# Performance work log

Measured on AMD Instinct MI355X. Metric: run time of the kernel, lower is better.

The kernel has to match this reference:

```python
import jax, jax.numpy as jnp
import numpy as np
import math

B, S, D, H = 2, 2048, 1024, 16
DK = D // H


def setup_inputs() -> dict:
    key = jax.random.key(0)
    ks = jax.random.split(key, 12)
    sc = 0.02
    inp = {
        "k": jax.random.normal(ks[0], (B, S, D), jnp.float32),
        "q": jax.random.normal(ks[1], (B, S, D), jnp.float32),
        "v": jax.random.normal(ks[2], (B, S, D), jnp.float32),
        "mask": 1,
        "w_k": jax.random.normal(ks[3], (D, D), jnp.float32) * sc,
        "b_k": jax.random.normal(ks[4], (D,), jnp.float32) * sc,
        "w_q": jax.random.normal(ks[5], (D, D), jnp.float32) * sc,
        "b_q": jax.random.normal(ks[6], (D,), jnp.float32) * sc,
        "w_v": jax.random.normal(ks[7], (D, D), jnp.float32) * sc,
        "b_v": jax.random.normal(ks[8], (D,), jnp.float32) * sc,
        "w_o": jax.random.normal(ks[9], (D, D), jnp.float32) * sc,
        "b_o": jax.random.normal(ks[10], (D,), jnp.float32) * sc,
    }
    return inp


def _mha(k, q, v, mask, w_k, b_k, w_q, b_q, w_v, b_v, w_o, b_o):
    # torch Linear: x @ W.T + b  (W is [out, in])
    key = k @ w_k.T + b_k
    query = q @ w_q.T + b_q
    value = v @ w_v.T + b_v
    # [B, S, D] -> [B, H, S, DK]
    key = key.reshape(B, S, H, DK).transpose(0, 2, 1, 3)
    query = query.reshape(B, S, H, DK).transpose(0, 2, 1, 3)
    value = value.reshape(B, S, H, DK).transpose(0, 2, 1, 3)
    # NOTE: original multiplies by sqrt(d_k) (not divides) -- faithful.
    scores = jnp.einsum("bhqd,bhkd->bhqk", query, key) * math.sqrt(DK)
    if mask:
        causal = jnp.triu(jnp.ones((S, S), dtype=bool), k=1)
        scores = jnp.where(causal, -jnp.inf, scores)
    # dropout p=0.0 is identity (original applies dropout to scores pre-softmax)
    attn = jax.nn.softmax(scores, axis=-1)
    out = jnp.einsum("bhqk,bhkd->bhqd", attn, value)
    out = out.transpose(0, 2, 1, 3).reshape(B, S, D)
    return out @ w_o.T + b_o


def reference(k, q, v, mask, w_k, b_k, w_q, b_q, w_v, b_v, w_o, b_o):
    return _mha(k, q, v, mask, w_k, b_k, w_q, b_q, w_v, b_v, w_o, b_o)
```

## Files before the change

kernel.cpp:

```cpp
#include <hip/hip_runtime.h>


typedef float f32x4 __attribute__((ext_vector_type(4)));
typedef float f32x16 __attribute__((ext_vector_type(16)));
typedef unsigned int u32x4 __attribute__((ext_vector_type(4)));
typedef _Float16 f16x8 __attribute__((ext_vector_type(8)));
typedef __fp16 fp16x2 __attribute__((ext_vector_type(2)));

#define DEV static __device__ __forceinline__

DEV unsigned short f2h(float x) {
  _Float16 h = (_Float16)x;
  union { _Float16 h; unsigned short u; } v; v.h = h;
  return v.u;
}

DEV unsigned pkrtz(float a, float b) {
  union { fp16x2 h; unsigned u; } v;
  v.h = __builtin_amdgcn_cvt_pkrtz(a, b);
  return v.u;
}

DEV float fexp2(float x) { return __builtin_amdgcn_exp2f(x); }

DEV void pswap(unsigned& a, unsigned& b) {
  auto r = __builtin_amdgcn_permlane32_swap(a, b, false, false);
  a = r[0]; b = r[1];
}

DEV void swap_pair(float v, float& x, float& y) {
  union { float f; unsigned u; } in; in.f = v;
  auto r = __builtin_amdgcn_permlane32_swap(in.u, in.u, false, false);
  union { unsigned u; float f; } ox, oy; ox.u = r[0]; oy.u = r[1];
  x = ox.f; y = oy.f;
}

DEV f16x8 mkfrag(unsigned a, unsigned b, unsigned c, unsigned d) {
  union { unsigned u[4]; f16x8 v; } z;
  z.u[0] = a; z.u[1] = b; z.u[2] = c; z.u[3] = d;
  return z.v;
}

DEV void mfma16(f32x4& d, u32x4 a, u32x4 b) {
  asm("v_mfma_f32_16x16x32_f16 %0, %1, %2, %0" : "+v"(d) : "v"(a), "v"(b));
}

DEV void gload16(const void* g, void* l) {
  __builtin_amdgcn_global_load_lds(
      (const __attribute__((address_space(1))) unsigned int*)g,
      (__attribute__((address_space(3))) unsigned int*)l, 16, 0, 0);
}

DEV u32x4 cvt8(float4 a, float4 b) {
  union { unsigned short us[8]; u32x4 v; } z;
  z.us[0] = f2h(a.x); z.us[1] = f2h(a.y); z.us[2] = f2h(a.z); z.us[3] = f2h(a.w);
  z.us[4] = f2h(b.x); z.us[5] = f2h(b.y); z.us[6] = f2h(b.z); z.us[7] = f2h(b.w);
  return z.v;
}

#define VMCNT0() asm volatile("s_waitcnt vmcnt(0)" ::: "memory")
#define LGKMCNT0() asm volatile("s_waitcnt lgkmcnt(0)" ::: "memory")
#define NOPG(a,b,c,d)  asm volatile("s_nop 7\n\ts_nop 7" : "+v"(a), "+v"(b), "+v"(c), "+v"(d))

__global__ __launch_bounds__(256) void cvt_w(
    const float* __restrict__ wk, const float* __restrict__ wq,
    const float* __restrict__ wv, const float* __restrict__ wo,
    unsigned short* __restrict__ dst) {
  const int i = (blockIdx.x * 256 + threadIdx.x) * 4;
  const float* src; int off;
  if (i < 1048576)      { src = wk; off = 0; }
  else if (i < 2097152) { src = wq; off = 1048576; }
  else if (i < 3145728) { src = wv; off = 2097152; }
  else                  { src = wo; off = 3145728; }
  float4 val = *(const float4*)(src + (i - off));
  ushort4 o;
  o.x = f2h(val.x); o.y = f2h(val.y); o.z = f2h(val.z); o.w = f2h(val.w);
  *(ushort4*)(dst + i) = o;
}

DEV void proj_body(const float* __restrict__ A, const unsigned short* __restrict__ W,
                   const float* __restrict__ bias, void* __restrict__ out, int mode,
                   float oscale, int m0, int n0) {
  __shared__ alignas(16) char lds_a[2][8192];
  __shared__ alignas(16) char lds_b[2][8192];
  const int t = threadIdx.x;
  const int l = t & 63, g = l >> 4, c = l & 15, w = t >> 6;
  const int wr = w >> 1, wc = w & 1;

  f32x4 acc[4][4] = {};

  const int i0 = t, i1 = t + 256;
  const int ar0 = i0 >> 2, as0 = (i0 & 3) ^ (ar0 & 3);
  const int ar1 = i1 >> 2, as1 = (i1 & 3) ^ (ar1 & 3);
  const float* gaf0 = A + (long)(m0 + ar0) * 1024 + as0 * 8;
  const float* gaf1 = A + (long)(m0 + ar1) * 1024 + as1 * 8;
  const unsigned short* gb0 = W + (long)(n0 + ar0) * 1024 + as0 * 8;
  const unsigned short* gb1 = W + (long)(n0 + ar1) * 1024 + as1 * 8;
  const int lo0 = i0 * 16, lo1 = i1 * 16;

  int aoff[4], boff[4];
#pragma unroll
  for (int i = 0; i < 4; i++) {
    const int ra = (wr << 6) + (i << 4) + c;
    aoff[i] = ra * 64 + ((g << 4) ^ ((ra & 3) << 4));
    const int rb = (wc << 6) + (i << 4) + c;
    boff[i] = rb * 64 + ((g << 4) ^ ((rb & 3) << 4));
  }

  float4 r0a = *(const float4*)(gaf0);
  float4 r0b = *(const float4*)(gaf0 + 4);
  float4 r1a = *(const float4*)(gaf1);
  float4 r1b = *(const float4*)(gaf1 + 4);
  gload16(gb0, lds_b[0] + lo0);
  gload16(gb1, lds_b[0] + lo1);

  for (int kt = 0; kt < 32; kt++) {
    const int cur = kt & 1;
    VMCNT0();
    *(u32x4*)(lds_a[cur] + lo0) = cvt8(r0a, r0b);
    *(u32x4*)(lds_a[cur] + lo1) = cvt8(r1a, r1b);
    if (kt + 1 < 32) {
      const int o = (kt + 1) << 5;
      r0a = *(const float4*)(gaf0 + o);
      r0b = *(const float4*)(gaf0 + o + 4);
      r1a = *(const float4*)(gaf1 + o);
      r1b = *(const float4*)(gaf1 + o + 4);
    }
    LGKMCNT0();
    __builtin_amdgcn_s_barrier();
    if (kt + 1 < 32) {
      gload16(gb0 + ((kt + 1) << 5), lds_b[cur ^ 1] + lo0);
      gload16(gb1 + ((kt + 1) << 5), lds_b[cur ^ 1] + lo1);
    }
    u32x4 af[4], bf[4];
#pragma unroll
    for (int i = 0; i < 4; i++) af[i] = *(const u32x4*)(lds_a[cur] + aoff[i]);
#pragma unroll
    for (int j = 0; j < 4; j++) bf[j] = *(const u32x4*)(lds_b[cur] + boff[j]);
#pragma unroll
    for (int i = 0; i < 4; i++)
#pragma unroll
      for (int j = 0; j < 4; j++)
        mfma16(acc[i][j], af[i], bf[j]);
  }

  NOPG(acc[0][0], acc[0][1], acc[0][2], acc[0][3]);
  NOPG(acc[1][0], acc[1][1], acc[1][2], acc[1][3]);
  NOPG(acc[2][0], acc[2][1], acc[2][2], acc[2][3]);
  NOPG(acc[3][0], acc[3][1], acc[3][2], acc[3][3]);

  if (mode == 1) {
#pragma unroll
    for (int j = 0; j < 4; j++) {
      const int n = n0 + (wc << 6) + (j << 4) + c;
      const float bb = bias[n];
      const int h = n >> 6, d = n & 63;
#pragma unroll
      for (int i = 0; i < 4; i++) {
        const int m = m0 + (wr << 6) + (i << 4) + (g << 2);
        const int b = m >> 11, s = m & 2047;
        ushort4 o;
        o.x = f2h(acc[i][j][0] + bb);
        o.y = f2h(acc[i][j][1] + bb);
        o.z = f2h(acc[i][j][2] + bb);
        o.w = f2h(acc[i][j][3] + bb);
        *(ushort4*)&((unsigned short*)out)[((long)((b << 4) + h) * 64 + d) * 2048 + s] = o;
      }
    }
  } else {
#pragma unroll
    for (int j = 0; j < 4; j++) {
      const int n = n0 + (wc << 6) + (j << 4) + c;
      const float bb = bias[n];
#pragma unroll
      for (int i = 0; i < 4; i++) {
#pragma unroll
        for (int r = 0; r < 4; r++) {
          const int m = m0 + (wr << 6) + (i << 4) + (g << 2) + r;
          const float val = (acc[i][j][r] + bb) * oscale;
          const int b = m >> 11, s = m & 2047;
          const int h = n >> 6, d = n & 63;
          ((unsigned short*)out)[((long)((b << 4) + h) * 2048 + s) * 64 + d] = f2h(val);
        }
      }
    }
  }
}

__global__ __launch_bounds__(256) void gemm_proj(
    const float* kf, const float* qf, const float* vf,
    const unsigned short* wkb, const unsigned short* wqb, const unsigned short* wvb,
    const float* bk, const float* bq, const float* bvv,
    unsigned short* Kp, unsigned short* Qp, unsigned short* VpT) {
  const int bid = blockIdx.x;
  const int n = bid / 96;
  const int gg = bid % 96;
  const int m = gg / 3;
  const int z = gg % 3;
  const float* A = (z == 0) ? kf : (z == 1) ? qf : vf;
  const unsigned short* W = (z == 0) ? wkb : (z == 1) ? wqb : wvb;
  const float* bias = (z == 0) ? bk : (z == 1) ? bq : bvv;
  void* out = (z == 0) ? (void*)Kp : (z == 1) ? (void*)Qp : (void*)VpT;
  const float sc = (z == 1) ? 11.5415603271f : 1.0f;
  proj_body(A, W, bias, out, (z == 2) ? 1 : 0, sc, m << 7, n << 7);
}

__global__ __launch_bounds__(256) void gemm_out(
    const unsigned short* __restrict__ A, const unsigned short* __restrict__ W,
    const float* __restrict__ bias, float* __restrict__ out) {
  __shared__ alignas(16) char lds_a[2][8192];
  __shared__ alignas(16) char lds_b[2][8192];
  const int t = threadIdx.x;
  const int l = t & 63, g = l >> 4, c = l & 15, w = t >> 6;
  const int wr = w >> 1, wc = w & 1;
  const int bid = blockIdx.x;
  const int m0 = (bid & 31) << 7, n0 = (bid >> 5) << 7;

  f32x4 acc[4][4] = {};

  const int i0 = t, i1 = t + 256;
  const int ar0 = i0 >> 2, as0 = (i0 & 3) ^ (ar0 & 3);
  const int ar1 = i1 >> 2, as1 = (i1 & 3) ^ (ar1 & 3);
  const unsigned short* ga0 = A + (long)(m0 + ar0) * 1024 + as0 * 8;
  const unsigned short* ga1 = A + (long)(m0 + ar1) * 1024 + as1 * 8;
  const unsigned short* gb0 = W + (long)(n0 + ar0) * 1024 + as0 * 8;
  const unsigned short* gb1 = W + (long)(n0 + ar1) * 1024 + as1 * 8;
  const int lo0 = i0 * 16, lo1 = i1 * 16;

  int aoff[4], boff[4];
#pragma unroll
  for (int i = 0; i < 4; i++) {
    const int ra = (wr << 6) + (i << 4) + c;
    aoff[i] = ra * 64 + ((g << 4) ^ ((ra & 3) << 4));
    const int rb = (wc << 6) + (i << 4) + c;
    boff[i] = rb * 64 + ((g << 4) ^ ((rb & 3) << 4));
  }

  gload16(ga0, lds_a[0] + lo0);
  gload16(ga1, lds_a[0] + lo1);
  gload16(gb0, lds_b[0] + lo0);
  gload16(gb1, lds_b[0] + lo1);

  for (int kt = 0; kt < 32; kt++) {
    const int cur = kt & 1;
    VMCNT0();
    __builtin_amdgcn_s_barrier();
    if (kt + 1 < 32) {
      gload16(ga0 + ((kt + 1) << 5), lds_a[cur ^ 1] + lo0);
      gload16(ga1 + ((kt + 1) << 5), lds_a[cur ^ 1] + lo1);
      gload16(gb0 + ((kt + 1) << 5), lds_b[cur ^ 1] + lo0);
      gload16(gb1 + ((kt + 1) << 5), lds_b[cur ^ 1] + lo1);
    }
    u32x4 af[4], bf[4];
#pragma unroll
    for (int i = 0; i < 4; i++) af[i] = *(const u32x4*)(lds_a[cur] + aoff[i]);
#pragma unroll
    for (int j = 0; j < 4; j++) bf[j] = *(const u32x4*)(lds_b[cur] + boff[j]);
#pragma unroll
    for (int i = 0; i < 4; i++)
#pragma unroll
      for (int j = 0; j < 4; j++)
        mfma16(acc[i][j], af[i], bf[j]);
  }

  NOPG(acc[0][0], acc[0][1], acc[0][2], acc[0][3]);
  NOPG(acc[1][0], acc[1][1], acc[1][2], acc[1][3]);
  NOPG(acc[2][0], acc[2][1], acc[2][2], acc[2][3]);
  NOPG(acc[3][0], acc[3][1], acc[3][2], acc[3][3]);

#pragma unroll
  for (int j = 0; j < 4; j++) {
    const int n = n0 + (wc << 6) + (j << 4) + c;
    const float bb = bias[n];
#pragma unroll
    for (int i = 0; i < 4; i++) {
#pragma unroll
      for (int r = 0; r < 4; r++) {
        const int m = m0 + (wr << 6) + (i << 4) + (g << 2) + r;
        out[(long)m * 1024 + n] = acc[i][j][r] + bb;
      }
    }
  }
}

__global__ __launch_bounds__(128) void attn_kernel(
    const unsigned short* __restrict__ Qp, const unsigned short* __restrict__ Kp,
    const unsigned short* __restrict__ VpT, unsigned short* __restrict__ O) {
  __shared__ alignas(16) char lds_k[2][8192];
  __shared__ alignas(16) char lds_v[2][8192];

  const int t = threadIdx.x;
  const int lane = t & 63, w = t >> 6;
  const int hi = lane >> 5, c32 = lane & 31;
  const int bh = blockIdx.x;
  const int qt = 31 - (int)blockIdx.y;
  const int qs = (qt << 6) + (w << 5);
  const int ntiles = qt + 1;

  const unsigned short* gk[4]; const unsigned short* gv[4]; int lofs[4];
#pragma unroll
  for (int n = 0; n < 4; n++) {
    const int idx = t + 128 * n;
    const int row = idx >> 3, sl = (idx & 7) ^ (row & 7);
    gk[n] = Kp + ((long)bh * 2048 + row) * 64 + sl * 8;
    gv[n] = VpT + ((long)bh * 64 + row) * 2048 + sl * 8;
    lofs[n] = idx * 16;
  }

  int koff[2][4];
#pragma unroll
  for (int x = 0; x < 2; x++)
#pragma unroll
    for (int y = 0; y < 4; y++) {
      const int row = 32 * x + c32;
      koff[x][y] = row * 128 + ((((y << 1) + hi) << 4) ^ ((row & 7) << 4));
    }

  const unsigned short* qrow = Qp + ((long)bh * 2048 + qs + c32) * 64 + hi * 8;
  f16x8 qf[4];
#pragma unroll
  for (int ks = 0; ks < 4; ks++) qf[ks] = *(const f16x8*)(qrow + ks * 16);

  f32x16 oT0 = {}, oT1 = {};
  float mrun = -1e30f, lrun = 0.f;
  const int qloc = (qs & 63) + c32;

#pragma unroll
  for (int n = 0; n < 4; n++) {
    gload16(gk[n], lds_k[0] + lofs[n]);
    gload16(gv[n], lds_v[0] + lofs[n]);
  }

  for (int tt = 0; tt < ntiles; tt++) {
    const int cur = tt & 1;
    VMCNT0();
    __builtin_amdgcn_s_barrier();
    if (tt + 1 < ntiles) {
      const long kvn = (long)(tt + 1) << 6;
#pragma unroll
      for (int n = 0; n < 4; n++) {
        gload16(gk[n] + kvn * 64, lds_k[cur ^ 1] + lofs[n]);
        gload16(gv[n] + kvn,      lds_v[cur ^ 1] + lofs[n]);
      }
    }

    f32x16 s0 = {}, s1 = {};
    __builtin_amdgcn_s_setprio(1);
#pragma unroll
    for (int ks = 0; ks < 4; ks++) {
      const f16x8 a0 = *(const f16x8*)(lds_k[cur] + koff[0][ks]);
      const f16x8 a1 = *(const f16x8*)(lds_k[cur] + koff[1][ks]);
      s0 = __builtin_amdgcn_mfma_f32_32x32x16_f16(a0, qf[ks], s0, 0, 0, 0);
      s1 = __builtin_amdgcn_mfma_f32_32x32x16_f16(a1, qf[ks], s1, 0, 0, 0);
    }
    __builtin_amdgcn_s_setprio(0);

    if (tt == qt) {
#pragma unroll
      for (int r = 0; r < 16; r++) {
        const int kvc = (r & 3) + 8 * (r >> 2) + 4 * hi;
        if (kvc > qloc)      s0[r] = -1e30f;
        if (kvc + 32 > qloc) s1[r] = -1e30f;
      }
    }

    float tm[16];
#pragma unroll
    for (int r = 0; r < 16; r++) tm[r] = fmaxf(s0[r], s1[r]);
#pragma unroll
    for (int d = 8; d >= 1; d >>= 1)
#pragma unroll
      for (int r = 0; r < 8; r++)
        if (r < d) tm[r] = fmaxf(tm[r], tm[r + d]);
    float x, y;
    swap_pair(tm[0], x, y);
    const float pmax = fmaxf(x, y);

    if (!__all(pmax - mrun <= 8.0f)) {
      const float mnew = fmaxf(mrun, pmax);
      const float corr = fexp2(mrun - mnew);
      mrun = mnew;
      lrun *= corr;
      oT0 *= corr;
      oT1 *= corr;
    }

#pragma unroll
    for (int r = 0; r < 16; r++) {
      s0[r] = fexp2(s0[r] - mrun);
      s1[r] = fexp2(s1[r] - mrun);
    }
    float ts[16];
#pragma unroll
    for (int r = 0; r < 16; r++) ts[r] = s0[r] + s1[r];
#pragma unroll
    for (int d = 8; d >= 1; d >>= 1)
#pragma unroll
      for (int r = 0; r < 8; r++)
        if (r < d) ts[r] = ts[r] + ts[r + d];
    lrun += ts[0];

    unsigned pk[8];
#pragma unroll
    for (int m = 0; m < 8; m++) pk[m] = pkrtz(s0[2 * m], s0[2 * m + 1]);
    pswap(pk[0], pk[2]); pswap(pk[1], pk[3]);
    pswap(pk[4], pk[6]); pswap(pk[5], pk[7]);
    const f16x8 pf0 = mkfrag(pk[0], pk[1], pk[2], pk[3]);
    const f16x8 pf1 = mkfrag(pk[4], pk[5], pk[6], pk[7]);
#pragma unroll
    for (int m = 0; m < 8; m++) pk[m] = pkrtz(s1[2 * m], s1[2 * m + 1]);
    pswap(pk[0], pk[2]); pswap(pk[1], pk[3]);
    pswap(pk[4], pk[6]); pswap(pk[5], pk[7]);
    const f16x8 pf2 = mkfrag(pk[0], pk[1], pk[2], pk[3]);
    const f16x8 pf3 = mkfrag(pk[4], pk[5], pk[6], pk[7]);

    __builtin_amdgcn_s_setprio(1);
    {
      const f16x8 v00 = *(const f16x8*)(lds_v[cur] + koff[0][0]);
      const f16x8 v01 = *(const f16x8*)(lds_v[cur] + koff[0][1]);
      const f16x8 v02 = *(const f16x8*)(lds_v[cur] + koff[0][2]);
      const f16x8 v03 = *(const f16x8*)(lds_v[cur] + koff[0][3]);
      oT0 = __builtin_amdgcn_mfma_f32_32x32x16_f16(v00, pf0, oT0, 0, 0, 0);
      oT0 = __builtin_amdgcn_mfma_f32_32x32x16_f16(v01, pf1, oT0, 0, 0, 0);
      oT0 = __builtin_amdgcn_mfma_f32_32x32x16_f16(v02, pf2, oT0, 0, 0, 0);
      oT0 = __builtin_amdgcn_mfma_f32_32x32x16_f16(v03, pf3, oT0, 0, 0, 0);
      const f16x8 v10 = *(const f16x8*)(lds_v[cur] + koff[1][0]);
      const f16x8 v11 = *(const f16x8*)(lds_v[cur] + koff[1][1]);
      const f16x8 v12 = *(const f16x8*)(lds_v[cur] + koff[1][2]);
      const f16x8 v13 = *(const f16x8*)(lds_v[cur] + koff[1][3]);
      oT1 = __builtin_amdgcn_mfma_f32_32x32x16_f16(v10, pf0, oT1, 0, 0, 0);
      oT1 = __builtin_amdgcn_mfma_f32_32x32x16_f16(v11, pf1, oT1, 0, 0, 0);
      oT1 = __builtin_amdgcn_mfma_f32_32x32x16_f16(v12, pf2, oT1, 0, 0, 0);
      oT1 = __builtin_amdgcn_mfma_f32_32x32x16_f16(v13, pf3, oT1, 0, 0, 0);
    }
    __builtin_amdgcn_s_setprio(0);
  }

  float sx, sy;
  swap_pair(lrun, sx, sy);
  const float inv = 1.0f / (sx + sy);
  const int b = bh >> 4, h = bh & 15;
  const long rowbase = ((long)b * 2048 + qs + c32) * 1024 + (h << 6);
#pragma unroll
  for (int dt = 0; dt < 2; dt++) {
#pragma unroll
    for (int g4 = 0; g4 < 4; g4++) {
      const f32x16& o = dt ? oT1 : oT0;
      uint2 pkd;
      pkd.x = pkrtz(o[4 * g4 + 0] * inv, o[4 * g4 + 1] * inv);
      pkd.y = pkrtz(o[4 * g4 + 2] * inv, o[4 * g4 + 3] * inv);
      *(uint2*)&O[rowbase + 32 * dt + 8 * g4 + 4 * hi] = pkd;
    }
  }
}

extern "C" void kernel_launch(void* const* d_in, const int* in_sizes, int n_in,
                              void* d_out, int out_size, void* d_ws, size_t ws_size,
                              hipStream_t stream) {
  (void)in_sizes; (void)n_in; (void)out_size; (void)ws_size;
  const float* kin = (const float*)d_in[0];
  const float* qin = (const float*)d_in[1];
  const float* vin = (const float*)d_in[2];
  const float* wk  = (const float*)d_in[4];
  const float* bk  = (const float*)d_in[5];
  const float* wq  = (const float*)d_in[6];
  const float* bq  = (const float*)d_in[7];
  const float* wv  = (const float*)d_in[8];
  const float* bv  = (const float*)d_in[9];
  const float* wo  = (const float*)d_in[10];
  const float* bo  = (const float*)d_in[11];

  unsigned short* ws  = (unsigned short*)d_ws;
  unsigned short* wkb = ws + 12582912;
  unsigned short* wqb = ws + 13631488;
  unsigned short* wvb = ws + 14680064;
  unsigned short* wob = ws + 15728640;
  unsigned short* Kp  = ws + 16777216;
  unsigned short* Qp  = ws + 20971520;
  unsigned short* VpT = ws + 25165824;
  unsigned short* Oo  = ws + 29360128;

  cvt_w<<<4096, 256, 0, stream>>>(wk, wq, wv, wo, wkb);
  gemm_proj<<<768, 256, 0, stream>>>(kin, qin, vin, wkb, wqb, wvb,
                                     bk, bq, bv, Kp, Qp, VpT);
  attn_kernel<<<dim3(32, 32), 128, 0, stream>>>(Qp, Kp, VpT, Oo);
  gemm_out<<<256, 256, 0, stream>>>(Oo, wob, bo, (float*)d_out);
}
```

Baseline: 119.0 us.

## Split attention KV range into two partitions and merge with log-sum-exp kernel

```diff
diff --git a/kernel.cpp b/kernel.cpp
--- a/kernel.cpp
+++ b/kernel.cpp
@@ -285,7 +285,9 @@
 
 __global__ __launch_bounds__(128) void attn_kernel(
     const unsigned short* __restrict__ Qp, const unsigned short* __restrict__ Kp,
-    const unsigned short* __restrict__ VpT, unsigned short* __restrict__ O) {
+    const unsigned short* __restrict__ VpT, unsigned short* __restrict__ O0,
+    unsigned short* __restrict__ O1, float2* __restrict__ ml0,
+    float2* __restrict__ ml1) {
   __shared__ alignas(16) char lds_k[2][8192];
   __shared__ alignas(16) char lds_v[2][8192];
 
@@ -294,8 +296,19 @@
   const int hi = lane >> 5, c32 = lane & 31;
   const int bh = blockIdx.x;
   const int qt = 31 - (int)blockIdx.y;
+  const int sp = blockIdx.z;
+  const int h0 = (qt + 2) >> 1;
+  const int tb = sp ? h0 : 0;
+  const int ntiles = sp ? (qt + 1 - h0) : h0;
   const int qs = (qt << 6) + (w << 5);
-  const int ntiles = qt + 1;
+
+  unsigned short* Op = sp ? O1 : O0;
+  float2* mlp = sp ? ml1 : ml0;
+
+  if (ntiles == 0) {
+    if (hi == 0) mlp[bh * 2048 + qs + c32] = make_float2(-1e30f, 0.0f);
+    return;
+  }
 
   const unsigned short* gk[4]; const unsigned short* gv[4]; int lofs[4];
 #pragma unroll
@@ -325,10 +338,13 @@
   float mrun = -1e30f, lrun = 0.f;
   const int qloc = (qs & 63) + c32;
 
-#pragma unroll
-  for (int n = 0; n < 4; n++) {
-    gload16(gk[n], lds_k[0] + lofs[n]);
-    gload16(gv[n], lds_v[0] + lofs[n]);
+  {
+    const long kb = (long)tb << 6;
+#pragma unroll
+    for (int n = 0; n < 4; n++) {
+      gload16(gk[n] + kb * 64, lds_k[0] + lofs[n]);
+      gload16(gv[n] + kb,      lds_v[0] + lofs[n]);
+    }
   }
 
   for (int tt = 0; tt < ntiles; tt++) {
@@ -336,7 +352,7 @@
     VMCNT0();
     __builtin_amdgcn_s_barrier();
     if (tt + 1 < ntiles) {
-      const long kvn = (long)(tt + 1) << 6;
+      const long kvn = (long)(tb + tt + 1) << 6;
 #pragma unroll
       for (int n = 0; n < 4; n++) {
         gload16(gk[n] + kvn * 64, lds_k[cur ^ 1] + lofs[n]);
@@ -355,7 +371,7 @@
     }
     __builtin_amdgcn_s_setprio(0);
 
-    if (tt == qt) {
+    if (tb + tt == qt) {
 #pragma unroll
       for (int r = 0; r < 16; r++) {
         const int kvc = (r & 3) + 8 * (r >> 2) + 4 * hi;
@@ -438,7 +454,8 @@
 
   float sx, sy;
   swap_pair(lrun, sx, sy);
-  const float inv = 1.0f / (sx + sy);
+  const float lsum = sx + sy;
+  const float inv = 1.0f / lsum;
   const int b = bh >> 4, h = bh & 15;
   const long rowbase = ((long)b * 2048 + qs + c32) * 1024 + (h << 6);
 #pragma unroll
@@ -449,9 +466,40 @@
       uint2 pkd;
       pkd.x = pkrtz(o[4 * g4 + 0] * inv, o[4 * g4 + 1] * inv);
       pkd.y = pkrtz(o[4 * g4 + 2] * inv, o[4 * g4 + 3] * inv);
-      *(uint2*)&O[rowbase + 32 * dt + 8 * g4 + 4 * hi] = pkd;
-    }
-  }
+      *(uint2*)&Op[rowbase + 32 * dt + 8 * g4 + 4 * hi] = pkd;
+    }
+  }
+  if (hi == 0) mlp[bh * 2048 + qs + c32] = make_float2(mrun, lsum);
+}
+
+__global__ __launch_bounds__(256) void merge_o(
+    unsigned short* __restrict__ O0, const unsigned short* __restrict__ O1,
+    const float2* __restrict__ ml0, const float2* __restrict__ ml1) {
+  const int idx = (blockIdx.x * 256 + threadIdx.x) * 8;
+  const int d = idx & 1023;
+  const int s = (idx >> 10) & 2047;
+  const int b = idx >> 21;
+  const int bh = (b << 4) + (d >> 6);
+  const float2 a = ml0[bh * 2048 + s];
+  const float2 c = ml1[bh * 2048 + s];
+  if (c.y == 0.0f) return;
+  const float M = fmaxf(a.x, c.x);
+  float w0 = a.y * fexp2(a.x - M);
+  float w1 = c.y * fexp2(c.x - M);
+  const float inv = 1.0f / (w0 + w1);
+  w0 *= inv; w1 *= inv;
+  const f16x8 o0 = *(const f16x8*)&O0[idx];
+  const f16x8 o1 = *(const f16x8*)&O1[idx];
+  uint4 r;
+  r.x = pkrtz(w0 * (float)o0[0] + w1 * (float)o1[0],
+              w0 * (float)o0[1] + w1 * (float)o1[1]);
+  r.y = pkrtz(w0 * (float)o0[2] + w1 * (float)o1[2],
+              w0 * (float)o0[3] + w1 * (float)o1[3]);
+  r.z = pkrtz(w0 * (float)o0[4] + w1 * (float)o1[4],
+              w0 * (float)o0[5] + w1 * (float)o1[5]);
+  r.w = pkrtz(w0 * (float)o0[6] + w1 * (float)o1[6],
+              w0 * (float)o0[7] + w1 * (float)o1[7]);
+  *(uint4*)&O0[idx] = r;
 }
 
 extern "C" void kernel_launch(void* const* d_in, const int* in_sizes, int n_in,
@@ -471,6 +519,9 @@
   const float* bo  = (const float*)d_in[11];
 
   unsigned short* ws  = (unsigned short*)d_ws;
+  unsigned short* O1  = ws;
+  float2* ml0 = (float2*)(ws + 4194304);
+  float2* ml1 = (float2*)(ws + 4456448);
   unsigned short* wkb = ws + 12582912;
   unsigned short* wqb = ws + 13631488;
   unsigned short* wvb = ws + 14680064;
@@ -483,6 +534,7 @@
   cvt_w<<<4096, 256, 0, stream>>>(wk, wq, wv, wo, wkb);
   gemm_proj<<<768, 256, 0, stream>>>(kin, qin, vin, wkb, wqb, wvb,
                                      bk, bq, bv, Kp, Qp, VpT);
-  attn_kernel<<<dim3(32, 32), 128, 0, stream>>>(Qp, Kp, VpT, Oo);
+  attn_kernel<<<dim3(32, 32, 2), 128, 0, stream>>>(Qp, Kp, VpT, Oo, O1, ml0, ml1);
+  merge_o<<<2048, 256, 0, stream>>>(Oo, O1, ml0, ml1);
   gemm_out<<<256, 256, 0, stream>>>(Oo, wob, bo, (float*)d_out);
 }
```

Result: faster. 115.2 us (median of 3 runs) (-3.2%).
